# Optimization experiments

Measured on AMD Instinct MI355X. Metric: run time of the kernel, lower is better.

The kernel has to match this reference:

```python
import jax, jax.numpy as jnp
import numpy as np
import math

PRE_D = 2048   # pre_d_model (scaled from 8192)
D = 4096       # d_model (scaled from 16384)
N = 64         # d_state (scaled from 128)
K = 4          # d_conv
EXP = 2
L = 128        # sequence_length
DI1 = EXP * PRE_D
DI2 = EXP * D
DTR1 = math.ceil(PRE_D / 16)
DTR2 = math.ceil(D / 16)


def _sinusoid(max_len, d):
    pe = np.zeros((max_len, d), np.float32)
    pos = np.arange(max_len, dtype=np.float32)[:, None]
    div = np.exp(np.arange(0, d, 2, dtype=np.float32) * (-math.log(10000.0) / d))
    pe[:, 0::2] = np.sin(pos * div)
    pe[:, 1::2] = np.cos(pos * div)
    return jnp.asarray(pe)


def _mamba_params(key, d_in, d_out, di, dtr, n, k):
    ks = jax.random.split(key, 6)
    s = 0.02
    dt = jnp.exp(jax.random.uniform(ks[4], (di,)) * (math.log(0.1) - math.log(1e-3)) + math.log(1e-3))
    return dict(
        in_proj=jax.random.normal(ks[0], (2 * di, d_in)) * s,
        conv_w=jax.random.normal(ks[1], (di, k)) * s,
        conv_b=jnp.zeros((di,)),
        x_proj=jax.random.normal(ks[2], (dtr + 2 * n, di)) * s,
        dt_w=jax.random.normal(ks[3], (di, dtr)) * s,
        dt_b=jnp.log(jnp.expm1(dt)),  # softplus^-1 of dt init
        A_log=jnp.log(jnp.tile(jnp.arange(1, n + 1, dtype=jnp.float32), (di, 1))),
        D=jnp.ones((di,)),
        out_proj=jax.random.normal(ks[5], (d_out, di)) * s,
    )


def setup_inputs() -> dict:
    key = jax.random.key(0)
    k1, k2, k3, k4 = jax.random.split(key, 4)
    inp = {
        'pe': _sinusoid(L, PRE_D),                              # (L, PRE_D)
        'to_cond_w': jax.random.normal(k3, (PRE_D, 1)) * 0.02,  # Linear(1 -> PRE_D)
        'to_cond_b': jnp.zeros((PRE_D,)),
        'condition': jax.random.normal(k4, (1,)),
        'batch': 1,
    }
    for pref, p in (('m1_', _mamba_params(k1, PRE_D, PRE_D, DI1, DTR1, N, K)),
                    ('m2_', _mamba_params(k2, PRE_D, D, DI2, DTR2, N, K))):
        for name, v in p.items():
            inp[pref + name] = v
    return inp


def _silu(x):
    return x * jax.nn.sigmoid(x)


def _mamba(x, in_w, cw, cb, xp_w, dt_w, dt_b, A_log, Dp, out_w, dtr, n):
    # x: (B, L, d_in)
    xz = x @ in_w.T                     # (B, L, 2*di)
    xr, z = jnp.split(xz, 2, axis=-1)
    kk = cw.shape[1]
    Lx = xr.shape[1]
    xpad = jnp.pad(xr, ((0, 0), (kk - 1, 0), (0, 0)))  # causal pad
    conv = sum(cw[:, i] * xpad[:, i:i + Lx, :] for i in range(kk)) + cb
    xr = _silu(conv)
    dbc = xr @ xp_w.T                   # (B, L, dtr + 2n)
    dt = dbc[..., :dtr]
    Bm = dbc[..., dtr:dtr + n]
    Cm = dbc[..., dtr + n:]
    dt = jax.nn.softplus(dt @ dt_w.T + dt_b)           # (B, L, di)
    A = -jnp.exp(A_log)                                 # (di, n)
    dA = jnp.exp(jnp.einsum('bld,dn->bldn', dt, A))
    dBx = jnp.einsum('bld,bln,bld->bldn', dt, Bm, xr)

    def comb(c1, c2):
        a1, b1 = c1
        a2, b2 = c2
        return a2 * a1, a2 * b1 + b2

    _, h = jax.lax.associative_scan(comb, (dA, dBx), axis=1)  # (B, L, di, n)
    y = jnp.einsum('bldn,bln->bld', h, Cm) + xr * Dp
    y = y * _silu(z)
    return y @ out_w.T


def reference(pe, to_cond_w, to_cond_b, condition,
              m1_in_proj, m1_conv_w, m1_conv_b, m1_x_proj, m1_dt_w, m1_dt_b, m1_A_log, m1_D, m1_out_proj,
              m2_in_proj, m2_conv_w, m2_conv_b, m2_x_proj, m2_dt_w, m2_dt_b, m2_A_log, m2_D, m2_out_proj,
              batch):
    cond = condition.reshape(-1, 1, 1)
    c = jnp.einsum('bli,oi->blo', cond, to_cond_w) + to_cond_b   # (Bc,1,PRE_D)
    x = jnp.tile(pe[None], (batch, 1, 1)) + c                    # (B, L, PRE_D)
    x = _mamba(x, m1_in_proj, m1_conv_w, m1_conv_b, m1_x_proj, m1_dt_w, m1_dt_b,
               m1_A_log, m1_D, m1_out_proj, DTR1, N)
    x = _mamba(x, m2_in_proj, m2_conv_w, m2_conv_b, m2_x_proj, m2_dt_w, m2_dt_b,
               m2_A_log, m2_D, m2_out_proj, DTR2, N)
    return x
```

## Files before the change

### kernel.cpp

```cpp
#include <hip/hip_runtime.h>
#include <hip/hip_bf16.h>
#include <math.h>


typedef __attribute__((ext_vector_type(8))) short short8_t;
typedef __attribute__((ext_vector_type(4))) float f32x4;

__device__ __forceinline__ float sigmoidf_(float x) {
  return 1.0f / (1.0f + __expf(-x));
}
__device__ __forceinline__ float softplusf_(float x) {
  return fmaxf(x, 0.0f) + log1pf(expf(-fabsf(x)));
}
__device__ __forceinline__ void splitbf(float f, ushort& h, ushort& lo) {
  __hip_bfloat16 hb = __float2bfloat16(f);
  h = *reinterpret_cast<ushort*>(&hb);
  float hf = __bfloat162float(hb);
  __hip_bfloat16 lb = __float2bfloat16(f - hf);
  lo = *reinterpret_cast<ushort*>(&lb);
}
__device__ __forceinline__ void tsplit(float f, ushort& h, ushort& lo) {
  unsigned u = __float_as_uint(f);
  h = (ushort)(u >> 16);
  float r = f - __uint_as_float(u & 0xFFFF0000u);
  lo = (ushort)(__float_as_uint(r) >> 16);
}
__device__ __forceinline__ size_t poff(int l, int d) {
  return (size_t)(d >> 5) * 8192 + (size_t)((d >> 3) & 3) * 1024 +
         (size_t)l * 8 + (d & 7);
}
__device__ __forceinline__ void g2l16(const float* g, float* lp) {
  __builtin_amdgcn_global_load_lds(
      (const __attribute__((address_space(1))) unsigned int*)g,
      (__attribute__((address_space(3))) unsigned int*)lp, 16, 0, 0);
}

__global__ __launch_bounds__(256) void k_prep(const float* __restrict__ pe,
                                              const float* __restrict__ cw,
                                              const float* __restrict__ cb,
                                              const float* __restrict__ cond,
                                              ushort* __restrict__ xp) {
  int i = blockIdx.x * 256 + threadIdx.x;
  int d = i & 2047;
  int l = i >> 11;
  float v = pe[i] + cond[0] * cw[d] + cb[d];
  ushort h, lo;
  splitbf(v, h, lo);
  size_t o = poff(l, d);
  xp[o] = h;
  xp[o + 4096] = lo;
}

#define KWS 32
__global__ __launch_bounds__(256, 3) void k_gemmW(const ushort* __restrict__ Ap,
                                                  const float* __restrict__ W, int ldw,
                                                  float* __restrict__ P,
                                                  int N, int Ks) {
  __shared__ float Wlds[2][128][32];

  const int n0   = blockIdx.x * 128;
  const int s    = blockIdx.z;
  const int kbeg = s * Ks;
  const int t    = threadIdx.x;
  const int l    = t & 63;
  const int w    = t >> 6;
  const int wm   = w >> 1;
  const int wn   = w & 1;
  const int lr   = l & 15;
  const int lg   = l >> 4;

  f32x4 acc[4][4];
#pragma unroll
  for (int mi = 0; mi < 4; ++mi)
#pragma unroll
    for (int ni = 0; ni < 4; ++ni) acc[mi][ni] = (f32x4)(0.0f);

  const int grow = l >> 3;
  const int gg   = (l & 7) ^ (grow & 7);
  const float* gW[4];
#pragma unroll
  for (int i = 0; i < 4; ++i)
    gW[i] = W + (size_t)(n0 + 8 * (w * 4 + i) + grow) * ldw + kbeg + gg * 4;

  const ushort* pA0 = Ap + (size_t)(kbeg >> 5) * 8192;
  const int arow = 64 * wm + lr;
  const int rsw  = lr & 7;

  const int nIter = Ks / KWS;

#pragma unroll
  for (int i = 0; i < 4; ++i)
    g2l16(gW[i], &Wlds[0][0][0] + (w * 4 + i) * 256);
  __syncthreads();

  for (int j = 0; j < nIter; ++j) {
    const int bi = j & 1;

    const ushort* pAj = pA0 + (size_t)j * 8192;
    short8_t ah[4], al[4];
#pragma unroll
    for (int mi = 0; mi < 4; ++mi) {
      const size_t fo = (size_t)lg * 1024 + (size_t)(arow + 16 * mi) * 8;
      ah[mi] = *(const short8_t*)(pAj + fo);
      al[mi] = *(const short8_t*)(pAj + 4096 + fo);
    }
    if (j + 1 < nIter) {
#pragma unroll
      for (int i = 0; i < 4; ++i)
        g2l16(gW[i] + (size_t)(j + 1) * KWS,
              &Wlds[bi ^ 1][0][0] + (w * 4 + i) * 256);
    }
    const float* Wb = &Wlds[bi][0][0];
#pragma unroll
    for (int ni = 0; ni < 4; ++ni) {
      const int r = 64 * wn + 16 * ni + lr;
      const float4 v0 = *(const float4*)(Wb + r * 32 + (((2 * lg) ^ rsw) * 4));
      const float4 v1 = *(const float4*)(Wb + r * 32 + (((2 * lg + 1) ^ rsw) * 4));
      short8_t bh, bl;
      {
        const float f8[8] = {v0.x, v0.y, v0.z, v0.w, v1.x, v1.y, v1.z, v1.w};
#pragma unroll
        for (int e = 0; e < 8; ++e) {
          ushort h, lo;
          tsplit(f8[e], h, lo);
          bh[e] = (short)h;
          bl[e] = (short)lo;
        }
      }
#pragma unroll
      for (int mi = 0; mi < 4; ++mi) {
        acc[mi][ni] = __builtin_amdgcn_mfma_f32_16x16x32_bf16(ah[mi], bh, acc[mi][ni], 0, 0, 0);
        acc[mi][ni] = __builtin_amdgcn_mfma_f32_16x16x32_bf16(al[mi], bh, acc[mi][ni], 0, 0, 0);
        acc[mi][ni] = __builtin_amdgcn_mfma_f32_16x16x32_bf16(ah[mi], bl, acc[mi][ni], 0, 0, 0);
      }
    }
    __syncthreads();
  }

  float* Pd = P + (size_t)s * 128 * N + n0 + 64 * wn;
#pragma unroll
  for (int mi = 0; mi < 4; ++mi)
#pragma unroll
    for (int ni = 0; ni < 4; ++ni) {
#pragma unroll
      for (int jj = 0; jj < 4; ++jj) {
        const int m = 64 * wm + 16 * mi + 4 * lg + jj;
        Pd[(size_t)m * N + 16 * ni + lr] = acc[mi][ni][jj];
      }
    }
}

#define KSTEP 32
__global__ __launch_bounds__(256, 2) void k_gemm(const ushort* __restrict__ Ap,
                                                 const float* __restrict__ W, int ldw,
                                                 float* __restrict__ P,
                                                 int N, int Ks) {
  __shared__ ushort Ws[2][2][4][128][8];

  const int n0   = blockIdx.x * 128;
  const int s    = blockIdx.z;
  const int kbeg = s * Ks;
  const int t    = threadIdx.x;
  const int l    = t & 63;
  const int w    = t >> 6;
  const int wm   = w >> 1;
  const int wn   = w & 1;
  const int lr   = l & 15;
  const int lg   = l >> 4;

  f32x4 acc[4][4];
#pragma unroll
  for (int mi = 0; mi < 4; ++mi)
#pragma unroll
    for (int ni = 0; ni < 4; ++ni) acc[mi][ni] = (f32x4)(0.0f);

  const int srow = t >> 3;
  const int sk16 = t & 7;
  const int skb  = sk16 >> 1;
  const int se0  = (sk16 & 1) * 4;
  const float* pWg = W + (size_t)(n0 + srow) * ldw + kbeg + sk16 * 4;

  const ushort* pAc = Ap + (size_t)(kbeg >> 5) * 8192;
  const int arow = 64 * wm + lr;
  const int brow = 64 * wn + lr;

  const int nIter = Ks / KSTEP;
  float4 wv[4];

#pragma unroll
  for (int r = 0; r < 4; ++r)
    wv[r] = *(const float4*)(pWg + (size_t)(r * 32) * ldw);
#pragma unroll
  for (int r = 0; r < 4; ++r) {
    ushort4 h4, l4;
    splitbf(wv[r].x, h4.x, l4.x); splitbf(wv[r].y, h4.y, l4.y);
    splitbf(wv[r].z, h4.z, l4.z); splitbf(wv[r].w, h4.w, l4.w);
    *(ushort4*)&Ws[0][0][skb][srow + 32 * r][se0] = h4;
    *(ushort4*)&Ws[0][1][skb][srow + 32 * r][se0] = l4;
  }
  __syncthreads();

  for (int j = 0; j < nIter; ++j) {
    const int bi = j & 1;
    const bool more = (j + 1 < nIter);

    const ushort* pAj = pAc + (size_t)j * 8192;
    short8_t ah[4], al[4];
#pragma unroll
    for (int mi = 0; mi < 4; ++mi) {
      const size_t fo = (size_t)lg * 1024 + (size_t)(arow + 16 * mi) * 8;
      ah[mi] = *(const short8_t*)(pAj + fo);
      al[mi] = *(const short8_t*)(pAj + 4096 + fo);
    }
    if (more) {
      const size_t ko = (size_t)(j + 1) * KSTEP;
#pragma unroll
      for (int r = 0; r < 4; ++r)
        wv[r] = *(const float4*)(pWg + ko + (size_t)(r * 32) * ldw);
    }
    short8_t bh[4], bl[4];
#pragma unroll
    for (int ni = 0; ni < 4; ++ni) {
      bh[ni] = *(const short8_t*)&Ws[bi][0][lg][brow + 16 * ni][0];
      bl[ni] = *(const short8_t*)&Ws[bi][1][lg][brow + 16 * ni][0];
    }
#pragma unroll
    for (int mi = 0; mi < 4; ++mi)
#pragma unroll
      for (int ni = 0; ni < 4; ++ni) {
        acc[mi][ni] = __builtin_amdgcn_mfma_f32_16x16x32_bf16(ah[mi], bh[ni], acc[mi][ni], 0, 0, 0);
        acc[mi][ni] = __builtin_amdgcn_mfma_f32_16x16x32_bf16(al[mi], bh[ni], acc[mi][ni], 0, 0, 0);
        acc[mi][ni] = __builtin_amdgcn_mfma_f32_16x16x32_bf16(ah[mi], bl[ni], acc[mi][ni], 0, 0, 0);
      }
    if (more) {
#pragma unroll
      for (int r = 0; r < 4; ++r) {
        ushort4 h4, l4;
        splitbf(wv[r].x, h4.x, l4.x); splitbf(wv[r].y, h4.y, l4.y);
        splitbf(wv[r].z, h4.z, l4.z); splitbf(wv[r].w, h4.w, l4.w);
        *(ushort4*)&Ws[bi ^ 1][0][skb][srow + 32 * r][se0] = h4;
        *(ushort4*)&Ws[bi ^ 1][1][skb][srow + 32 * r][se0] = l4;
      }
    }
    __syncthreads();
  }

  float* Pd = P + (size_t)s * 128 * N + n0 + 64 * wn;
#pragma unroll
  for (int mi = 0; mi < 4; ++mi)
#pragma unroll
    for (int ni = 0; ni < 4; ++ni) {
#pragma unroll
      for (int jj = 0; jj < 4; ++jj) {
        const int m = 64 * wm + 16 * mi + 4 * lg + jj;
        Pd[(size_t)m * N + 16 * ni + lr] = acc[mi][ni][jj];
      }
    }
}

__global__ __launch_bounds__(256) void k_reduce(const float* __restrict__ P,
                                                float* __restrict__ Y,
                                                ushort* __restrict__ Yp,
                                                int MN, int N, int S, int ep,
                                                const float* __restrict__ bias) {
  int i = (blockIdx.x * 256 + threadIdx.x) * 4;
  if (i >= MN) return;
  float4 v = *(const float4*)&P[i];
  for (int s = 1; s < S; ++s) {
    float4 p = *(const float4*)&P[(size_t)s * MN + i];
    v.x += p.x; v.y += p.y; v.z += p.z; v.w += p.w;
  }
  int n = i % N;
  int l = i / N;
  if (ep & 1) {
    const float4 b = *(const float4*)&bias[n];
    v.x = softplusf_(v.x + b.x);
    v.y = softplusf_(v.y + b.y);
    v.z = softplusf_(v.z + b.z);
    v.w = softplusf_(v.w + b.w);
  }
  if (ep & 4) *(float4*)&Y[i] = v;
  if (ep & 2) {
    ushort4 h4, l4;
    splitbf(v.x, h4.x, l4.x);
    splitbf(v.y, h4.y, l4.y);
    splitbf(v.z, h4.z, l4.z);
    splitbf(v.w, h4.w, l4.w);
    size_t o = poff(l, n);
    *(ushort4*)&Yp[o] = h4;
    *(ushort4*)&Yp[o + 4096] = l4;
  }
}

__global__ __launch_bounds__(256) void k_reduceA(const float* __restrict__ P,
                                                 float* __restrict__ Y, int MN) {
  int g = blockIdx.y;
  int i = (blockIdx.x * 256 + threadIdx.x) * 4;
  if (i >= MN) return;
  const float* Pp = P + (size_t)g * 8 * MN;
  float4 v = *(const float4*)&Pp[i];
  for (int s = 1; s < 8; ++s) {
    float4 p = *(const float4*)&Pp[(size_t)s * MN + i];
    v.x += p.x; v.y += p.y; v.z += p.z; v.w += p.w;
  }
  *(float4*)&Y[(size_t)g * MN + i] = v;
}

__global__ __launch_bounds__(256) void k_conv_silu(const float* __restrict__ xz,
                                                   const float* __restrict__ cw,
                                                   const float* __restrict__ cb,
                                                   float* __restrict__ xc,
                                                   ushort* __restrict__ xcp,
                                                   int DI, int lg2DI) {
  int i = blockIdx.x * 256 + threadIdx.x;
  int l = i >> lg2DI;
  int d = i & (DI - 1);
  const float4 w = *(const float4*)&cw[d * 4];
  const float* xr = xz + d;
  int ld = 2 * DI;
  float s = cb[d];
  s += w.w * xr[l * ld];
  if (l >= 1) s += w.z * xr[(l - 1) * ld];
  if (l >= 2) s += w.y * xr[(l - 2) * ld];
  if (l >= 3) s += w.x * xr[(l - 3) * ld];
  float v = s * sigmoidf_(s);
  xc[i] = v;
  ushort h, lo;
  splitbf(v, h, lo);
  size_t o = poff(l, d);
  xcp[o] = h;
  xcp[o + 4096] = lo;
}

__global__ __launch_bounds__(256) void k_scan(const float* __restrict__ dt,
                                              const float* __restrict__ xc,
                                              const float* __restrict__ dbc,
                                              const float* __restrict__ A_log,
                                              const float* __restrict__ Dp,
                                              float* __restrict__ y,
                                              int DI, int DTR) {
  __shared__ float cs[4][32][65];
  const int wid = threadIdx.x >> 6;
  const int n   = threadIdx.x & 63;
  const int d   = blockIdx.x * 4 + wid;
  const int du  = __builtin_amdgcn_readfirstlane(d);
  const float A  = -__expf(A_log[(size_t)du * 64 + n]);
  const float Dd = Dp[du];
  const int ldbc = DTR + 128;
  const float* Bp = dbc + DTR + n;
  const float* Cp = dbc + DTR + 64 + n;
  float h = 0.0f;
  for (int l0 = 0; l0 < 128; l0 += 32) {
#pragma unroll 8
    for (int l = l0; l < l0 + 32; ++l) {
      float dtv = dt[(size_t)l * DI + du];
      float xcv = xc[(size_t)l * DI + du];
      float dA  = __expf(dtv * A);
      float bx  = dtv * xcv;
      h = fmaf(dA, h, bx * Bp[(size_t)l * ldbc]);
      cs[wid][l - l0][n] = h * Cp[(size_t)l * ldbc];
    }
    __syncthreads();
    const int r = n & 31, hf = n >> 5;
    float ssum = 0.0f;
#pragma unroll
    for (int j = 0; j < 32; ++j) ssum += cs[wid][r][hf * 32 + j];
    ssum += __shfl_xor(ssum, 32, 64);
    if (n < 32) {
      int ll = l0 + r;
      float xcv = xc[(size_t)ll * DI + du];
      y[(size_t)ll * DI + du] = ssum + xcv * Dd;
    }
    __syncthreads();
  }
}

__global__ __launch_bounds__(256) void k_gate(const float* __restrict__ yb,
                                              const float* __restrict__ xz,
                                              ushort* __restrict__ yp,
                                              int DI, int lg2DI) {
  int i = blockIdx.x * 256 + threadIdx.x;
  int l = i >> lg2DI;
  int d = i & (DI - 1);
  float z = xz[((size_t)l << (lg2DI + 1)) + DI + d];
  float v = yb[i] * (z * sigmoidf_(z));
  ushort h, lo;
  splitbf(v, h, lo);
  size_t o = poff(l, d);
  yp[o] = h;
  yp[o + 4096] = lo;
}

struct GemmCtx {
  float* part;
  float* part2;
  long long cap;
};

static inline void reduce_stage(float* dstF, ushort* dstP, int N, int S, int ep,
                                const float* bias, const GemmCtx& cx,
                                hipStream_t stream) {
  const int MN = 128 * N;
  const int rb = (MN / 4 + 255) / 256;
  if (S <= 16) {
    k_reduce<<<rb, 256, 0, stream>>>(cx.part, dstF, dstP, MN, N, S, ep, bias);
  } else {
    k_reduceA<<<dim3(rb, S / 8), 256, 0, stream>>>(cx.part, cx.part2, MN);
    k_reduce<<<rb, 256, 0, stream>>>(cx.part2, dstF, dstP, MN, N, S / 8, ep, bias);
  }
}

static inline void gemmS(const ushort* Ap, const float* W, int ldw,
                         float* dstF, ushort* dstP,
                         int N, int K, int Sdes, int ep,
                         const float* bias, const GemmCtx& cx, hipStream_t stream) {
  int S = Sdes;
  if (S > K / KSTEP) S = K / KSTEP;
  if (S < 1) S = 1;
  while (S > 1 && (long long)S * 128 * N > cx.cap) S >>= 1;
  const int Ks = K / S;
  const bool direct = (S == 1 && ep == 4);
  dim3 g(N / 128, 1, S);
  k_gemm<<<g, 256, 0, stream>>>(Ap, W, ldw, direct ? dstF : cx.part, N, Ks);
  if (!direct) reduce_stage(dstF, dstP, N, S, ep, bias, cx, stream);
}

static inline void gemmW(const ushort* Ap, const float* W, int ldw,
                         float* dstF, ushort* dstP,
                         int N, int K, int Sdes, int ep,
                         const float* bias, const GemmCtx& cx, hipStream_t stream) {
  int S = Sdes;
  if (S > K / KWS) S = K / KWS;
  if (S < 1) S = 1;
  while (S > 1 && (long long)S * 128 * N > cx.cap) S >>= 1;
  const int Ks = K / S;
  const bool direct = (S == 1 && ep == 4);
  dim3 g(N / 128, 1, S);
  k_gemmW<<<g, 256, 0, stream>>>(Ap, W, ldw, direct ? dstF : cx.part, N, Ks);
  if (!direct) reduce_stage(dstF, dstP, N, S, ep, bias, cx, stream);
}

extern "C" void kernel_launch(void* const* d_in, const int* in_sizes, int n_in,
                              void* d_out, int out_size, void* d_ws, size_t ws_size,
                              hipStream_t stream) {
  const float* pe        = (const float*)d_in[0];
  const float* to_cond_w = (const float*)d_in[1];
  const float* to_cond_b = (const float*)d_in[2];
  const float* condition = (const float*)d_in[3];
  const int o = (in_sizes[4] == 1) ? 5 : 4;
  const float* m1_in_proj  = (const float*)d_in[o + 0];
  const float* m1_conv_w   = (const float*)d_in[o + 1];
  const float* m1_conv_b   = (const float*)d_in[o + 2];
  const float* m1_x_proj   = (const float*)d_in[o + 3];
  const float* m1_dt_w     = (const float*)d_in[o + 4];
  const float* m1_dt_b     = (const float*)d_in[o + 5];
  const float* m1_A_log    = (const float*)d_in[o + 6];
  const float* m1_D        = (const float*)d_in[o + 7];
  const float* m1_out_proj = (const float*)d_in[o + 8];
  const float* m2_in_proj  = (const float*)d_in[o + 9];
  const float* m2_conv_w   = (const float*)d_in[o + 10];
  const float* m2_conv_b   = (const float*)d_in[o + 11];
  const float* m2_x_proj   = (const float*)d_in[o + 12];
  const float* m2_dt_w     = (const float*)d_in[o + 13];
  const float* m2_dt_b     = (const float*)d_in[o + 14];
  const float* m2_A_log    = (const float*)d_in[o + 15];
  const float* m2_D        = (const float*)d_in[o + 16];
  const float* m2_out_proj = (const float*)d_in[o + 17];

  float* ws = (float*)d_ws;
  float*  xz   = ws;
  float*  xc   = ws + 2097152;
  float*  dbc  = ws + 3145728;
  float*  dtb  = ws + 3194880;
  float*  yb   = ws + 4243456;
  ushort* x0p  = (ushort*)(ws + 5292032);
  ushort* xcp  = (ushort*)(ws + 5554176);
  ushort* dbcp = (ushort*)(ws + 6602752);
  ushort* ybp  = (ushort*)(ws + 6651904);
  ushort* midp = (ushort*)(ws + 7700480);
  float*  part2 = ws + 7962624;
  float*  part  = ws + 8749056;

  GemmCtx cx;
  cx.part = part;
  cx.part2 = part2;
  cx.cap = (long long)(ws_size / 4) - 8749056;
  if (cx.cap < 0) cx.cap = 0;

  k_prep<<<1024, 256, 0, stream>>>(pe, to_cond_w, to_cond_b, condition, x0p);

  gemmW(x0p, m1_in_proj, 2048, xz, nullptr, 8192, 2048, 8, 4, nullptr, cx, stream);
  k_conv_silu<<<(128 * 4096) / 256, 256, 0, stream>>>(xz, m1_conv_w, m1_conv_b,
                                                      xc, xcp, 4096, 12);
  gemmS(xcp, m1_x_proj, 4096, dbc, dbcp, 256, 4096, 128, 6, nullptr, cx, stream);
  gemmS(dbcp, m1_dt_w, 128, dtb, nullptr, 4096, 128, 4, 5, m1_dt_b, cx, stream);
  k_scan<<<1024, 256, 0, stream>>>(dtb, xc, dbc, m1_A_log, m1_D, yb, 4096, 128);
  k_gate<<<(128 * 4096) / 256, 256, 0, stream>>>(yb, xz, ybp, 4096, 12);
  gemmW(ybp, m1_out_proj, 4096, nullptr, midp, 2048, 4096, 32, 2, nullptr, cx, stream);

  gemmW(midp, m2_in_proj, 2048, xz, nullptr, 16384, 2048, 4, 4, nullptr, cx, stream);
  k_conv_silu<<<(128 * 8192) / 256, 256, 0, stream>>>(xz, m2_conv_w, m2_conv_b,
                                                      xc, xcp, 8192, 13);
  gemmS(xcp, m2_x_proj, 8192, dbc, dbcp, 384, 8192, 128, 6, nullptr, cx, stream);
  gemmS(dbcp, m2_dt_w, 256, dtb, nullptr, 8192, 256, 4, 5, m2_dt_b, cx, stream);
  k_scan<<<2048, 256, 0, stream>>>(dtb, xc, dbc, m2_A_log, m2_D, yb, 8192, 256);
  k_gate<<<(128 * 8192) / 256, 256, 0, stream>>>(yb, xz, ybp, 8192, 13);
  gemmW(ybp, m2_out_proj, 8192, (float*)d_out, nullptr, 4096, 8192, 16, 4, nullptr, cx, stream);
}
```

Before: 352.4 us.

## Restructure k_gemmW into per-wave W slices with M split and staggered K start

k_gemmW now tiles the 128 M rows across two blocks (blockIdx.y), and each wave owns a private 32-row W slice in LDS. This removes the block-wide __syncthreads in favour of per-wave s_waitcnt on the async loads. K iteration starts at a block-dependent offset so blocks read different W columns at the same moment, and occupancy is raised to 4 blocks. Split-K factors for the out_proj GEMMs are halved to balance the doubled grid. Each W tile is now loaded by both M blocks, and correctness relies on each wave reading only its own LDS slice.

```diff
diff --git a/kernel.cpp b/kernel.cpp
--- a/kernel.cpp
+++ b/kernel.cpp
@@ -52,70 +52,74 @@
 }
 
 #define KWS 32
-__global__ __launch_bounds__(256, 3) void k_gemmW(const ushort* __restrict__ Ap,
+__global__ __launch_bounds__(256, 4) void k_gemmW(const ushort* __restrict__ Ap,
                                                   const float* __restrict__ W, int ldw,
                                                   float* __restrict__ P,
                                                   int N, int Ks) {
-  __shared__ float Wlds[2][128][32];
+  __shared__ float Wlds[2][4][32][32];
 
   const int n0   = blockIdx.x * 128;
+  const int m0   = blockIdx.y * 64;
   const int s    = blockIdx.z;
   const int kbeg = s * Ks;
   const int t    = threadIdx.x;
   const int l    = t & 63;
   const int w    = t >> 6;
-  const int wm   = w >> 1;
-  const int wn   = w & 1;
   const int lr   = l & 15;
   const int lg   = l >> 4;
 
-  f32x4 acc[4][4];
+  f32x4 acc[4][2];
 #pragma unroll
   for (int mi = 0; mi < 4; ++mi)
 #pragma unroll
-    for (int ni = 0; ni < 4; ++ni) acc[mi][ni] = (f32x4)(0.0f);
+    for (int ni = 0; ni < 2; ++ni) acc[mi][ni] = (f32x4)(0.0f);
 
   const int grow = l >> 3;
   const int gg   = (l & 7) ^ (grow & 7);
   const float* gW[4];
 #pragma unroll
   for (int i = 0; i < 4; ++i)
-    gW[i] = W + (size_t)(n0 + 8 * (w * 4 + i) + grow) * ldw + kbeg + gg * 4;
+    gW[i] = W + (size_t)(n0 + 32 * w + 8 * i + grow) * ldw + kbeg + gg * 4;
 
   const ushort* pA0 = Ap + (size_t)(kbeg >> 5) * 8192;
-  const int arow = 64 * wm + lr;
-  const int rsw  = lr & 7;
-
   const int nIter = Ks / KWS;
+  const int j0 = (blockIdx.x * 3 + blockIdx.y * 5 + s) % nIter;
 
 #pragma unroll
   for (int i = 0; i < 4; ++i)
-    g2l16(gW[i], &Wlds[0][0][0] + (w * 4 + i) * 256);
-  __syncthreads();
+    g2l16(gW[i] + (size_t)j0 * KWS, &Wlds[0][w][8 * i][0]);
 
   for (int j = 0; j < nIter; ++j) {
     const int bi = j & 1;
-
-    const ushort* pAj = pA0 + (size_t)j * 8192;
+    const int cur = (j0 + j) % nIter;
+    const bool more = (j + 1 < nIter);
+
+    const ushort* pAj = pA0 + (size_t)cur * 8192;
     short8_t ah[4], al[4];
 #pragma unroll
     for (int mi = 0; mi < 4; ++mi) {
-      const size_t fo = (size_t)lg * 1024 + (size_t)(arow + 16 * mi) * 8;
+      const size_t fo = (size_t)lg * 1024 + (size_t)(m0 + 16 * mi + lr) * 8;
       ah[mi] = *(const short8_t*)(pAj + fo);
       al[mi] = *(const short8_t*)(pAj + 4096 + fo);
     }
-    if (j + 1 < nIter) {
+    __builtin_amdgcn_sched_barrier(0);
+    if (more) {
+      const int nxt = (j0 + j + 1) % nIter;
 #pragma unroll
       for (int i = 0; i < 4; ++i)
-        g2l16(gW[i] + (size_t)(j + 1) * KWS,
-              &Wlds[bi ^ 1][0][0] + (w * 4 + i) * 256);
-    }
-    const float* Wb = &Wlds[bi][0][0];
-#pragma unroll
-    for (int ni = 0; ni < 4; ++ni) {
-      const int r = 64 * wn + 16 * ni + lr;
-      const float4 v0 = *(const float4*)(Wb + r * 32 + (((2 * lg) ^ rsw) * 4));
-      const float4 v1 = *(const float4*)(Wb + r * 32 + (((2 * lg + 1) ^ rsw) * 4));
+        g2l16(gW[i] + (size_t)nxt * KWS, &Wlds[bi ^ 1][w][8 * i][0]);
+      asm volatile("s_waitcnt vmcnt(4)" ::: "memory");
+    } else {
+      asm volatile("s_waitcnt vmcnt(0)" ::: "memory");
+    }
+    __builtin_amdgcn_sched_barrier(0);
+    const float* Wb = &Wlds[bi][w][0][0];
+#pragma unroll
+    for (int ni = 0; ni < 2; ++ni) {
+      const int r32 = 16 * ni + lr;
+      const int rsw = r32 & 7;
+      const float4 v0 = *(const float4*)(Wb + r32 * 32 + (((2 * lg) ^ rsw) * 4));
+      const float4 v1 = *(const float4*)(Wb + r32 * 32 + (((2 * lg + 1) ^ rsw) * 4));
       short8_t bh, bl;
       {
         const float f8[8] = {v0.x, v0.y, v0.z, v0.w, v1.x, v1.y, v1.z, v1.w};
@@ -134,17 +138,16 @@
         acc[mi][ni] = __builtin_amdgcn_mfma_f32_16x16x32_bf16(ah[mi], bl, acc[mi][ni], 0, 0, 0);
       }
     }
-    __syncthreads();
-  }
-
-  float* Pd = P + (size_t)s * 128 * N + n0 + 64 * wn;
+  }
+
+  float* Pd = P + (size_t)s * 128 * N + n0 + 32 * w;
 #pragma unroll
   for (int mi = 0; mi < 4; ++mi)
 #pragma unroll
-    for (int ni = 0; ni < 4; ++ni) {
+    for (int ni = 0; ni < 2; ++ni) {
 #pragma unroll
       for (int jj = 0; jj < 4; ++jj) {
-        const int m = 64 * wm + 16 * mi + 4 * lg + jj;
+        const int m = m0 + 16 * mi + 4 * lg + jj;
         Pd[(size_t)m * N + 16 * ni + lr] = acc[mi][ni][jj];
       }
     }
@@ -435,7 +438,7 @@
   while (S > 1 && (long long)S * 128 * N > cx.cap) S >>= 1;
   const int Ks = K / S;
   const bool direct = (S == 1 && ep == 4);
-  dim3 g(N / 128, 1, S);
+  dim3 g(N / 128, 2, S);
   k_gemmW<<<g, 256, 0, stream>>>(Ap, W, ldw, direct ? dstF : cx.part, N, Ks);
   if (!direct) reduce_stage(dstF, dstP, N, S, ep, bias, cx, stream);
 }
@@ -496,7 +499,7 @@
   gemmS(dbcp, m1_dt_w, 128, dtb, nullptr, 4096, 128, 4, 5, m1_dt_b, cx, stream);
   k_scan<<<1024, 256, 0, stream>>>(dtb, xc, dbc, m1_A_log, m1_D, yb, 4096, 128);
   k_gate<<<(128 * 4096) / 256, 256, 0, stream>>>(yb, xz, ybp, 4096, 12);
-  gemmW(ybp, m1_out_proj, 4096, nullptr, midp, 2048, 4096, 32, 2, nullptr, cx, stream);
+  gemmW(ybp, m1_out_proj, 4096, nullptr, midp, 2048, 4096, 16, 2, nullptr, cx, stream);
 
   gemmW(midp, m2_in_proj, 2048, xz, nullptr, 16384, 2048, 4, 4, nullptr, cx, stream);
   k_conv_silu<<<(128 * 8192) / 256, 256, 0, stream>>>(xz, m2_conv_w, m2_conv_b,
@@ -505,5 +508,5 @@
   gemmS(dbcp, m2_dt_w, 256, dtb, nullptr, 8192, 256, 4, 5, m2_dt_b, cx, stream);
   k_scan<<<2048, 256, 0, stream>>>(dtb, xc, dbc, m2_A_log, m2_D, yb, 8192, 256);
   k_gate<<<(128 * 8192) / 256, 256, 0, stream>>>(yb, xz, ybp, 8192, 13);
-  gemmW(ybp, m2_out_proj, 8192, (float*)d_out, nullptr, 4096, 8192, 16, 4, nullptr, cx, stream);
-}
+  gemmW(ybp, m2_out_proj, 8192, (float*)d_out, nullptr, 4096, 8192, 8, 4, nullptr, cx, stream);
+}
```

Measured after the change: 372.8 us. 1.06x slower.
